# Performance work log

Hardware: AMD Instinct MI355X
Metric: run time of the kernel (lower is better)

The kernel has to match this reference:

```python
import jax, jax.numpy as jnp
import numpy as np

EPS = 1e-7  # keras backend.epsilon()
KSZ = 3
STRIDE = 1
NUM_CAPS = 32        # output capsule types
NUM_CAPS_IN = 32     # input capsule types
POSE = 4             # 4x4 pose matrices
ROUTINGS = 3


def _patches(t, k, s):
    # t: [B, H, W, C] -> [B, Ho, Wo, k*k, C], patch index order i*k+j (row-major),
    # matching the tf depthwise_conv2d tile-filter trick + transpose in the source.
    B, H, W, C = t.shape
    Ho = (H - k) // s + 1
    Wo = (W - k) // s + 1
    return jnp.stack(
        [t[:, i:i + Ho * s:s, j:j + Wo * s:s, :] for i in range(k) for j in range(k)],
        axis=3,
    )


def setup_inputs() -> dict:
    key = jax.random.key(0)
    k1, k2, k3, k4 = jax.random.split(key, 4)
    B, H, W = 2, 14, 14
    KKI = KSZ * KSZ * NUM_CAPS_IN  # 288
    x = jax.random.normal(k1, (B, H, W, NUM_CAPS_IN, POSE * POSE + 1), dtype=jnp.float32)
    Wt = jax.random.normal(k2, (KKI, NUM_CAPS, POSE, POSE), dtype=jnp.float32) * 0.05
    beta_v = jax.random.normal(k3, (1, 1, 1, 1, NUM_CAPS, 1), dtype=jnp.float32) * 0.1
    beta_a = jax.random.normal(k4, (1, 1, 1, 1, NUM_CAPS, 1), dtype=jnp.float32) * 0.1
    return {"x": x, "W": Wt, "beta_v": beta_v, "beta_a": beta_a}


def _em_routing(V, a_i, beta_v, beta_a):
    # V: [B,Ho,Wo,KKI,NC,PP], a_i: [B,Ho,Wo,KKI,1,1]
    KKI, NC = V.shape[3], V.shape[4]
    R = jnp.full((KKI, NC, 1), 1.0 / NC, dtype=V.dtype)
    M_j = a_j = None
    for it in range(ROUTINGS):
        inv_temp = 1.0 + (min(ROUTINGS, 3.0) - 1.0) * it / max(1.0, ROUTINGS - 1.0)
        # --- maximization ---
        Rw = R * a_i                                    # [B,Ho,Wo,KKI,NC,1]
        Rsum = jnp.sum(Rw, axis=-3, keepdims=True)      # [B,Ho,Wo,1,NC,1]
        M_jk = jnp.sum(Rw * V, axis=-3, keepdims=True) / Rsum   # [B,Ho,Wo,1,NC,PP]
        # NOTE: source uses R_ij_sum (not R_ij) inside the variance sum; keep faithful.
        stdv = jnp.sqrt(jnp.sum(Rsum * jnp.square(V - M_jk), axis=-3, keepdims=True) / Rsum)
        cost_h = (beta_v + jnp.log(stdv + EPS)) * Rsum
        cost = jnp.sum(cost_h, axis=-1, keepdims=True)          # [B,Ho,Wo,1,NC,1]
        c_mean = jnp.mean(cost, axis=-2, keepdims=True)
        c_stdv = jnp.sqrt(jnp.sum(jnp.square(cost - c_mean), axis=-2, keepdims=True) / NC)
        a_cost = beta_a + (c_mean - cost) / (c_stdv + EPS)
        a_jk = jax.nn.sigmoid(inv_temp * a_cost)                # [B,Ho,Wo,1,NC,1]
        a_j = jnp.squeeze(jnp.squeeze(a_jk, axis=-3), axis=-1)  # [B,Ho,Wo,NC]
        M_j = jnp.squeeze(M_jk, axis=-3)                        # [B,Ho,Wo,NC,PP]
        if it < ROUTINGS - 1:
            # --- estimation ---
            log_a = jnp.log(a_j[..., None, :, None] + EPS)      # [B,Ho,Wo,1,NC,1]
            log_p = (log_a
                     - jnp.sum(jnp.square(V - M_jk) / (2.0 * jnp.square(stdv)), axis=-1, keepdims=True)
                     - jnp.sum(jnp.log(stdv + EPS), axis=-1, keepdims=True))
            R = jax.nn.softmax(log_p, axis=-2)                  # softmax over NC axis
    return M_j, a_j


def reference(x, W, beta_v, beta_a):
    B, H, Wd, Cin, _ = x.shape
    PP = POSE * POSE
    M_i = x[..., :PP]          # [B,H,W,Cin,16]
    a_i = x[..., PP]           # [B,H,W,Cin]
    # depthwise-conv patch extraction (conv path)
    Mp = _patches(M_i.reshape(B, H, Wd, Cin * PP), KSZ, STRIDE)   # [B,Ho,Wo,9,Cin*16]
    B_, Ho, Wo = Mp.shape[0], Mp.shape[1], Mp.shape[2]
    KKI = KSZ * KSZ * Cin
    Mp = Mp.reshape(B, Ho, Wo, KKI, POSE, POSE)
    ap = _patches(a_i, KSZ, STRIDE).reshape(B, Ho, Wo, KKI)
    # spatial transform: vote matrices V_ij = M_i @ W_ij
    V = jnp.einsum('bhwipq,icqr->bhwicpr', Mp, W)                 # [B,Ho,Wo,KKI,NC,4,4]
    V = V.reshape(B, Ho, Wo, KKI, NUM_CAPS, PP)
    a_in = ap[..., None, None]                                    # [B,Ho,Wo,KKI,1,1]
    M_j, a_j = _em_routing(V, a_in, beta_v, beta_a)
    # assemble output: [B,Ho,Wo,NC,16] poses concat sigmoid activation
    out = jnp.concatenate([M_j, jax.nn.sigmoid(a_j)[..., None]], axis=-1)
    return out  # [B,Ho,Wo,NC,17]
```

## Files before the change

### kernel.cpp

```cpp
#include <hip/hip_runtime.h>
#include <math.h>


#define EPSF 1e-7f
#define KKI 288
#define NC 32
#define NTHREADS 512
#define NSUB 16
#define IPT 18

__global__ __launch_bounds__(NTHREADS)
void caps_em_kernel(const float* __restrict__ x, const float* __restrict__ Wg,
                    const float* __restrict__ beta_v, const float* __restrict__ beta_a,
                    float* __restrict__ out)
{
    __shared__ float MpL[KKI * 16];
    __shared__ float apL[KKI];
    __shared__ float T1L[NC * 16];
    __shared__ float S1L[NC * 16];
    __shared__ float S2L[NC * 16];
    __shared__ float RsumL[NC];
    __shared__ float ML[NC * 17];
    __shared__ float I2L[NC * 17];
    __shared__ float constL[NC];
    __shared__ float aoutL[NC];

    const int t = threadIdx.x;
    const int bid = blockIdx.x;
    const int b = bid / 144;
    const int rem = bid - b * 144;
    const int ho = rem / 12;
    const int wo = rem - ho * 12;

    const int c = t & 31;
    const int isub = t >> 5;

    for (int idx = t; idx < KKI * 17; idx += NTHREADS) {
        int i = idx / 17;
        int e = idx - i * 17;
        int p = i >> 5, cin = i & 31;
        int di = p / 3, dj = p - di * 3;
        float vx = x[(((b * 14 + (ho + di)) * 14 + (wo + dj)) * 32 + cin) * 17 + e];
        if (e < 16) MpL[i * 16 + e] = vx; else apL[i] = vx;
    }
    for (int idx = t; idx < NC * 16; idx += NTHREADS) { T1L[idx] = 0.f; S1L[idx] = 0.f; S2L[idx] = 0.f; }
    if (t < NC) RsumL[t] = 0.f;
    __syncthreads();

    auto stats = [&](float inv_temp) {
        if (t < NC) {
            int cc = t;
            float rsum = RsumL[cc];
            float inv_rsum = 1.f / rsum;
            float bv = beta_v[cc];
            float cost = 0.f, slog = 0.f;
            #pragma unroll
            for (int d = 0; d < 16; ++d) {
                float m = T1L[cc * 16 + d] * inv_rsum;
                float var = S2L[cc * 16 + d] - 2.f * m * S1L[cc * 16 + d] + 288.f * m * m;
                var = fmaxf(var, 0.f);
                float stdv = sqrtf(var);
                float lg = logf(stdv + EPSF);
                slog += lg;
                cost += bv + lg;
                ML[cc * 17 + d] = m;
                I2L[cc * 17 + d] = 0.5f / var;
            }
            cost *= rsum;
            float csum = cost;
            csum += __shfl_xor(csum, 16); csum += __shfl_xor(csum, 8);
            csum += __shfl_xor(csum, 4);  csum += __shfl_xor(csum, 2);
            csum += __shfl_xor(csum, 1);
            float c_mean = csum * 0.03125f;
            float diff = cost - c_mean;
            float dsq = diff * diff;
            dsq += __shfl_xor(dsq, 16); dsq += __shfl_xor(dsq, 8);
            dsq += __shfl_xor(dsq, 4);  dsq += __shfl_xor(dsq, 2);
            dsq += __shfl_xor(dsq, 1);
            float c_stdv = sqrtf(dsq * 0.03125f);
            float a_cost = beta_a[cc] + (c_mean - cost) / (c_stdv + EPSF);
            float a_j = 1.f / (1.f + expf(-inv_temp * a_cost));
            constL[cc] = logf(a_j + EPSF) - slog;
            aoutL[cc] = 1.f / (1.f + expf(-a_j));
        }
    };

    {
        float t1[16], s1[16], s2[16];
        #pragma unroll
        for (int d = 0; d < 16; ++d) { t1[d] = 0.f; s1[d] = 0.f; s2[d] = 0.f; }
        float rsum = 0.f;
        for (int j = 0; j < IPT; ++j) {
            int i = isub * IPT + j;
            float a_i = apL[i];
            const float4* w4 = (const float4*)(Wg + (size_t)(i * NC + c) * 16);
            float wa[16], ma[16];
            ((float4*)wa)[0] = w4[0]; ((float4*)wa)[1] = w4[1];
            ((float4*)wa)[2] = w4[2]; ((float4*)wa)[3] = w4[3];
            const float4* mp4 = (const float4*)(MpL + i * 16);
            ((float4*)ma)[0] = mp4[0]; ((float4*)ma)[1] = mp4[1];
            ((float4*)ma)[2] = mp4[2]; ((float4*)ma)[3] = mp4[3];
            float v[16];
            #pragma unroll
            for (int p = 0; p < 4; ++p)
                #pragma unroll
                for (int r = 0; r < 4; ++r) {
                    float acc = ma[p * 4 + 0] * wa[0 * 4 + r];
                    acc = fmaf(ma[p * 4 + 1], wa[1 * 4 + r], acc);
                    acc = fmaf(ma[p * 4 + 2], wa[2 * 4 + r], acc);
                    acc = fmaf(ma[p * 4 + 3], wa[3 * 4 + r], acc);
                    v[p * 4 + r] = acc;
                }
            float rw = a_i * 0.03125f;
            rsum += rw;
            #pragma unroll
            for (int d = 0; d < 16; ++d) {
                t1[d] = fmaf(rw, v[d], t1[d]);
                s1[d] += v[d];
                s2[d] = fmaf(v[d], v[d], s2[d]);
            }
        }
        rsum += __shfl_xor(rsum, 32);
        #pragma unroll
        for (int d = 0; d < 16; ++d) {
            t1[d] += __shfl_xor(t1[d], 32);
            s1[d] += __shfl_xor(s1[d], 32);
            s2[d] += __shfl_xor(s2[d], 32);
        }
        if ((t & 32) == 0) {
            atomicAdd(&RsumL[c], rsum);
            #pragma unroll
            for (int d = 0; d < 16; ++d) {
                atomicAdd(&T1L[c * 16 + d], t1[d]);
                atomicAdd(&S1L[c * 16 + d], s1[d]);
                atomicAdd(&S2L[c * 16 + d], s2[d]);
            }
        }
        __syncthreads();
        stats(1.0f);
        __syncthreads();
    }

    for (int it = 1; it < 3; ++it) {
        float Mreg[16], i2[16];
        #pragma unroll
        for (int d = 0; d < 16; ++d) { Mreg[d] = ML[c * 17 + d]; i2[d] = I2L[c * 17 + d]; }
        float Kc = constL[c];
        for (int idx = t; idx < NC * 16; idx += NTHREADS) T1L[idx] = 0.f;
        if (t < NC) RsumL[t] = 0.f;
        __syncthreads();

        float t1[16];
        #pragma unroll
        for (int d = 0; d < 16; ++d) t1[d] = 0.f;
        float rsum = 0.f;
        for (int j = 0; j < IPT; ++j) {
            int i = isub * IPT + j;
            float a_i = apL[i];
            const float4* w4 = (const float4*)(Wg + (size_t)(i * NC + c) * 16);
            float wa[16], ma[16];
            ((float4*)wa)[0] = w4[0]; ((float4*)wa)[1] = w4[1];
            ((float4*)wa)[2] = w4[2]; ((float4*)wa)[3] = w4[3];
            const float4* mp4 = (const float4*)(MpL + i * 16);
            ((float4*)ma)[0] = mp4[0]; ((float4*)ma)[1] = mp4[1];
            ((float4*)ma)[2] = mp4[2]; ((float4*)ma)[3] = mp4[3];
            float v[16];
            #pragma unroll
            for (int p = 0; p < 4; ++p)
                #pragma unroll
                for (int r = 0; r < 4; ++r) {
                    float acc = ma[p * 4 + 0] * wa[0 * 4 + r];
                    acc = fmaf(ma[p * 4 + 1], wa[1 * 4 + r], acc);
                    acc = fmaf(ma[p * 4 + 2], wa[2 * 4 + r], acc);
                    acc = fmaf(ma[p * 4 + 3], wa[3 * 4 + r], acc);
                    v[p * 4 + r] = acc;
                }
            float lp = Kc;
            #pragma unroll
            for (int d = 0; d < 16; ++d) {
                float df = v[d] - Mreg[d];
                lp = fmaf(-df * df, i2[d], lp);
            }
            float mx = lp;
            mx = fmaxf(mx, __shfl_xor(mx, 16)); mx = fmaxf(mx, __shfl_xor(mx, 8));
            mx = fmaxf(mx, __shfl_xor(mx, 4));  mx = fmaxf(mx, __shfl_xor(mx, 2));
            mx = fmaxf(mx, __shfl_xor(mx, 1));
            float ex = expf(lp - mx);
            float s = ex;
            s += __shfl_xor(s, 16); s += __shfl_xor(s, 8);
            s += __shfl_xor(s, 4);  s += __shfl_xor(s, 2);
            s += __shfl_xor(s, 1);
            float r = ex / s;
            float rw = r * a_i;
            rsum += rw;
            #pragma unroll
            for (int d = 0; d < 16; ++d) t1[d] = fmaf(rw, v[d], t1[d]);
        }
        rsum += __shfl_xor(rsum, 32);
        #pragma unroll
        for (int d = 0; d < 16; ++d) t1[d] += __shfl_xor(t1[d], 32);
        if ((t & 32) == 0) {
            atomicAdd(&RsumL[c], rsum);
            #pragma unroll
            for (int d = 0; d < 16; ++d) atomicAdd(&T1L[c * 16 + d], t1[d]);
        }
        __syncthreads();
        stats(1.0f + (float)it);
        __syncthreads();
    }

    for (int idx = t; idx < NC * 17; idx += NTHREADS) {
        int cc = idx / 17;
        int e = idx - cc * 17;
        float val = (e < 16) ? ML[cc * 17 + e] : aoutL[cc];
        out[(size_t)bid * (NC * 17) + idx] = val;
    }
}

extern "C" void kernel_launch(void* const* d_in, const int* in_sizes, int n_in,
                              void* d_out, int out_size, void* d_ws, size_t ws_size,
                              hipStream_t stream) {
    const float* x  = (const float*)d_in[0];
    const float* W  = (const float*)d_in[1];
    const float* bv = (const float*)d_in[2];
    const float* ba = (const float*)d_in[3];
    float* out = (float*)d_out;
    caps_em_kernel<<<288, NTHREADS, 0, stream>>>(x, W, bv, ba, out);
}
```

Measured before the change: 208.2 us.

## Double threads per block, prefetch W, use fast math, pad shared accumulators

After: 282.7 us. 35.8% more time.

```diff
diff --git a/kernel.cpp b/kernel.cpp
--- a/kernel.cpp
+++ b/kernel.cpp
@@ -5,9 +5,11 @@
 #define EPSF 1e-7f
 #define KKI 288
 #define NC 32
-#define NTHREADS 512
-#define NSUB 16
-#define IPT 18
+#define NTHREADS 1024
+#define NSUB 32
+#define IPT 9
+
+__device__ __forceinline__ float frcp(float x) { return __builtin_amdgcn_rcpf(x); }
 
 __global__ __launch_bounds__(NTHREADS)
 void caps_em_kernel(const float* __restrict__ x, const float* __restrict__ Wg,
@@ -16,9 +18,9 @@
 {
     __shared__ float MpL[KKI * 16];
     __shared__ float apL[KKI];
-    __shared__ float T1L[NC * 16];
-    __shared__ float S1L[NC * 16];
-    __shared__ float S2L[NC * 16];
+    __shared__ float T1L[NC * 17];
+    __shared__ float S1L[NC * 17];
+    __shared__ float S2L[NC * 17];
     __shared__ float RsumL[NC];
     __shared__ float ML[NC * 17];
     __shared__ float I2L[NC * 17];
@@ -43,7 +45,7 @@
         float vx = x[(((b * 14 + (ho + di)) * 14 + (wo + dj)) * 32 + cin) * 17 + e];
         if (e < 16) MpL[i * 16 + e] = vx; else apL[i] = vx;
     }
-    for (int idx = t; idx < NC * 16; idx += NTHREADS) { T1L[idx] = 0.f; S1L[idx] = 0.f; S2L[idx] = 0.f; }
+    for (int idx = t; idx < NC * 17; idx += NTHREADS) { T1L[idx] = 0.f; S1L[idx] = 0.f; S2L[idx] = 0.f; }
     if (t < NC) RsumL[t] = 0.f;
     __syncthreads();
 
@@ -51,20 +53,20 @@
         if (t < NC) {
             int cc = t;
             float rsum = RsumL[cc];
-            float inv_rsum = 1.f / rsum;
+            float inv_rsum = frcp(rsum);
             float bv = beta_v[cc];
             float cost = 0.f, slog = 0.f;
             #pragma unroll
             for (int d = 0; d < 16; ++d) {
-                float m = T1L[cc * 16 + d] * inv_rsum;
-                float var = S2L[cc * 16 + d] - 2.f * m * S1L[cc * 16 + d] + 288.f * m * m;
+                float m = T1L[cc * 17 + d] * inv_rsum;
+                float var = S2L[cc * 17 + d] - 2.f * m * S1L[cc * 17 + d] + 288.f * m * m;
                 var = fmaxf(var, 0.f);
-                float stdv = sqrtf(var);
-                float lg = logf(stdv + EPSF);
+                float stdv = __fsqrt_rn(var);
+                float lg = __logf(stdv + EPSF);
                 slog += lg;
                 cost += bv + lg;
                 ML[cc * 17 + d] = m;
-                I2L[cc * 17 + d] = 0.5f / var;
+                I2L[cc * 17 + d] = 0.5f * frcp(var);
             }
             cost *= rsum;
             float csum = cost;
@@ -77,26 +79,36 @@
             dsq += __shfl_xor(dsq, 16); dsq += __shfl_xor(dsq, 8);
             dsq += __shfl_xor(dsq, 4);  dsq += __shfl_xor(dsq, 2);
             dsq += __shfl_xor(dsq, 1);
-            float c_stdv = sqrtf(dsq * 0.03125f);
-            float a_cost = beta_a[cc] + (c_mean - cost) / (c_stdv + EPSF);
-            float a_j = 1.f / (1.f + expf(-inv_temp * a_cost));
-            constL[cc] = logf(a_j + EPSF) - slog;
-            aoutL[cc] = 1.f / (1.f + expf(-a_j));
+            float c_stdv = __fsqrt_rn(dsq * 0.03125f);
+            float a_cost = beta_a[cc] + (c_mean - cost) * frcp(c_stdv + EPSF);
+            float a_j = frcp(1.f + __expf(-inv_temp * a_cost));
+            constL[cc] = __logf(a_j + EPSF) - slog;
+            aoutL[cc] = frcp(1.f + __expf(-a_j));
         }
     };
+
+    const float* wbase = Wg + (size_t)((isub * IPT) * NC + c) * 16;
 
     {
         float t1[16], s1[16], s2[16];
         #pragma unroll
         for (int d = 0; d < 16; ++d) { t1[d] = 0.f; s1[d] = 0.f; s2[d] = 0.f; }
         float rsum = 0.f;
+        float4 w0, w1, w2, w3;
+        {
+            const float4* wp = (const float4*)wbase;
+            w0 = wp[0]; w1 = wp[1]; w2 = wp[2]; w3 = wp[3];
+        }
         for (int j = 0; j < IPT; ++j) {
             int i = isub * IPT + j;
             float a_i = apL[i];
-            const float4* w4 = (const float4*)(Wg + (size_t)(i * NC + c) * 16);
+            int jn = (j + 1 < IPT) ? j + 1 : j;
+            const float4* wpn = (const float4*)(wbase + (size_t)jn * NC * 16);
+            float4 nw0 = wpn[0], nw1 = wpn[1], nw2 = wpn[2], nw3 = wpn[3];
+
             float wa[16], ma[16];
-            ((float4*)wa)[0] = w4[0]; ((float4*)wa)[1] = w4[1];
-            ((float4*)wa)[2] = w4[2]; ((float4*)wa)[3] = w4[3];
+            ((float4*)wa)[0] = w0; ((float4*)wa)[1] = w1;
+            ((float4*)wa)[2] = w2; ((float4*)wa)[3] = w3;
             const float4* mp4 = (const float4*)(MpL + i * 16);
             ((float4*)ma)[0] = mp4[0]; ((float4*)ma)[1] = mp4[1];
             ((float4*)ma)[2] = mp4[2]; ((float4*)ma)[3] = mp4[3];
@@ -119,6 +131,7 @@
                 s1[d] += v[d];
                 s2[d] = fmaf(v[d], v[d], s2[d]);
             }
+            w0 = nw0; w1 = nw1; w2 = nw2; w3 = nw3;
         }
         rsum += __shfl_xor(rsum, 32);
         #pragma unroll
@@ -131,9 +144,9 @@
             atomicAdd(&RsumL[c], rsum);
             #pragma unroll
             for (int d = 0; d < 16; ++d) {
-                atomicAdd(&T1L[c * 16 + d], t1[d]);
-                atomicAdd(&S1L[c * 16 + d], s1[d]);
-                atomicAdd(&S2L[c * 16 + d], s2[d]);
+                atomicAdd(&T1L[c * 17 + d], t1[d]);
+                atomicAdd(&S1L[c * 17 + d], s1[d]);
+                atomicAdd(&S2L[c * 17 + d], s2[d]);
             }
         }
         __syncthreads();
@@ -146,7 +159,7 @@
         #pragma unroll
         for (int d = 0; d < 16; ++d) { Mreg[d] = ML[c * 17 + d]; i2[d] = I2L[c * 17 + d]; }
         float Kc = constL[c];
-        for (int idx = t; idx < NC * 16; idx += NTHREADS) T1L[idx] = 0.f;
+        for (int idx = t; idx < NC * 17; idx += NTHREADS) T1L[idx] = 0.f;
         if (t < NC) RsumL[t] = 0.f;
         __syncthreads();
 
@@ -154,13 +167,21 @@
         #pragma unroll
         for (int d = 0; d < 16; ++d) t1[d] = 0.f;
         float rsum = 0.f;
+        float4 w0, w1, w2, w3;
+        {
+            const float4* wp = (const float4*)wbase;
+            w0 = wp[0]; w1 = wp[1]; w2 = wp[2]; w3 = wp[3];
+        }
         for (int j = 0; j < IPT; ++j) {
             int i = isub * IPT + j;
             float a_i = apL[i];
-            const float4* w4 = (const float4*)(Wg + (size_t)(i * NC + c) * 16);
+            int jn = (j + 1 < IPT) ? j + 1 : j;
+            const float4* wpn = (const float4*)(wbase + (size_t)jn * NC * 16);
+            float4 nw0 = wpn[0], nw1 = wpn[1], nw2 = wpn[2], nw3 = wpn[3];
+
             float wa[16], ma[16];
-            ((float4*)wa)[0] = w4[0]; ((float4*)wa)[1] = w4[1];
-            ((float4*)wa)[2] = w4[2]; ((float4*)wa)[3] = w4[3];
+            ((float4*)wa)[0] = w0; ((float4*)wa)[1] = w1;
+            ((float4*)wa)[2] = w2; ((float4*)wa)[3] = w3;
             const float4* mp4 = (const float4*)(MpL + i * 16);
             ((float4*)ma)[0] = mp4[0]; ((float4*)ma)[1] = mp4[1];
             ((float4*)ma)[2] = mp4[2]; ((float4*)ma)[3] = mp4[3];
@@ -185,16 +206,17 @@
             mx = fmaxf(mx, __shfl_xor(mx, 16)); mx = fmaxf(mx, __shfl_xor(mx, 8));
             mx = fmaxf(mx, __shfl_xor(mx, 4));  mx = fmaxf(mx, __shfl_xor(mx, 2));
             mx = fmaxf(mx, __shfl_xor(mx, 1));
-            float ex = expf(lp - mx);
+            float ex = __expf(lp - mx);
             float s = ex;
             s += __shfl_xor(s, 16); s += __shfl_xor(s, 8);
             s += __shfl_xor(s, 4);  s += __shfl_xor(s, 2);
             s += __shfl_xor(s, 1);
-            float r = ex / s;
+            float r = ex * frcp(s);
             float rw = r * a_i;
             rsum += rw;
             #pragma unroll
             for (int d = 0; d < 16; ++d) t1[d] = fmaf(rw, v[d], t1[d]);
+            w0 = nw0; w1 = nw1; w2 = nw2; w3 = nw3;
         }
         rsum += __shfl_xor(rsum, 32);
         #pragma unroll
@@ -202,7 +224,7 @@
         if ((t & 32) == 0) {
             atomicAdd(&RsumL[c], rsum);
             #pragma unroll
-            for (int d = 0; d < 16; ++d) atomicAdd(&T1L[c * 16 + d], t1[d]);
+            for (int d = 0; d < 16; ++d) atomicAdd(&T1L[c * 17 + d], t1[d]);
         }
         __syncthreads();
         stats(1.0f + (float)it);
```
